# Kernel optimization log

Measured on AMD Instinct MI355X. Metric: run time of the kernel, lower is better.

## Reference

```python
import jax, jax.numpy as jnp
import numpy as np

N = 100000          # nodes
E = 1600000         # edges (nnz of A)
D_IN = 128
D_OUT = 128


def setup_inputs() -> dict:
    key = jax.random.key(0)
    ks = jax.random.split(key, 9)
    s = 1.0 / np.sqrt(D_IN)
    inp = {
        "h_n": jax.random.normal(ks[0], (N, D_IN), dtype=jnp.float32),
        "W_w": jax.random.uniform(ks[1], (D_OUT, D_IN), jnp.float32, -s, s),
        "W_b": jax.random.uniform(ks[2], (D_OUT,), jnp.float32, -s, s),
        "Wt_w": jax.random.uniform(ks[3], (D_OUT, D_IN), jnp.float32, -s, s),
        "Wt_b": jax.random.uniform(ks[4], (D_OUT,), jnp.float32, -s, s),
        "Ws_w": jax.random.uniform(ks[5], (D_OUT, D_IN), jnp.float32, -s, s),
        "Ws_b": jax.random.uniform(ks[6], (D_OUT,), jnp.float32, -s, s),
        # COO indices of sparse adjacency A (binary values): A[rows[e], cols[e]] = 1
        "rows": jax.random.randint(ks[7], (E,), 0, N, dtype=jnp.int64)
                if jax.config.jax_enable_x64 else
                jax.random.randint(ks[7], (E,), 0, N, dtype=jnp.int32),
        "cols": jax.random.randint(ks[8], (E,), 0, N, dtype=jnp.int32),
    }
    inp["rows"] = inp["rows"].astype(jnp.int32)
    return inp


def reference(h_n, W_w, W_b, Wt_w, Wt_b, Ws_w, Ws_b, rows, cols):
    # Dense projections: [N, D_OUT]
    Wh  = h_n @ W_w.T + W_b    # W(h_n)
    Wth = h_n @ Wt_w.T + Wt_b  # W_trans(h_n)
    Wsh = h_n @ Ws_w.T + Ws_b  # W_self(h_n)

    # A @ Wh  : out[i] = sum over edges (i=rows[e], j=cols[e]) of Wh[j]
    agg   = jax.ops.segment_sum(Wh[cols],  rows, num_segments=N)
    # A_T @ Wth : out[i] = sum over edges (j=rows[e], i=cols[e]) of Wth[j]
    agg_t = jax.ops.segment_sum(Wth[rows], cols, num_segments=N)

    # exact (erf-based) GELU, matching torch F.gelu default
    return jax.nn.gelu(agg + agg_t + Wsh, approximate=False)
```

## Files before the change

### kernel.cpp

```cpp
#include <hip/hip_runtime.h>


typedef __bf16 bf16;
typedef __bf16 bf16x2 __attribute__((ext_vector_type(2)));
typedef __bf16 bf16x4 __attribute__((ext_vector_type(4)));
typedef __bf16 bf16x8 __attribute__((ext_vector_type(8)));
typedef float  f32x4  __attribute__((ext_vector_type(4)));
typedef unsigned int u32;

#define D 128
#define BKT_CAP 2432
#define BIN_CHUNK 2048

__global__ void k_cast(const float* __restrict__ src, bf16* __restrict__ dst, int n4) {
    int i = blockIdx.x * 256 + threadIdx.x;
    if (i < n4) {
        f32x4 v = *(const f32x4*)&src[i * 4];
        bf16x4 o;
        o.x = (bf16)v.x; o.y = (bf16)v.y; o.z = (bf16)v.z; o.w = (bf16)v.w;
        *(bf16x4*)&dst[i * 4] = o;
    }
}

__global__ __launch_bounds__(256) void k_bin(
    const int* __restrict__ rows, const int* __restrict__ cols,
    int* __restrict__ gcnt_f, int* __restrict__ gcnt_r,
    u32* __restrict__ buf_f, u32* __restrict__ buf_r, int E, int B) {
    __shared__ int hf[1024], hr[1024];
    int t = threadIdx.x;
    int base = blockIdx.x * BIN_CHUNK;
    for (int b = t; b < B; b += 256) { hf[b] = 0; hr[b] = 0; }
    __syncthreads();
    int r[8], c[8];
#pragma unroll
    for (int i = 0; i < 8; ++i) {
        int e = base + i * 256 + t;
        if (e < E) {
            r[i] = rows[e]; c[i] = cols[e];
            atomicAdd(&hf[r[i] >> 7], 1);
            atomicAdd(&hr[c[i] >> 7], 1);
        }
    }
    __syncthreads();
    for (int b = t; b < B; b += 256) {
        int v = hf[b]; if (v) hf[b] = atomicAdd(&gcnt_f[b], v);
        int w = hr[b]; if (w) hr[b] = atomicAdd(&gcnt_r[b], w);
    }
    __syncthreads();
#pragma unroll
    for (int i = 0; i < 8; ++i) {
        int e = base + i * 256 + t;
        if (e < E) {
            int p = atomicAdd(&hf[r[i] >> 7], 1);
            if (p < BKT_CAP)
                buf_f[(size_t)(r[i] >> 7) * BKT_CAP + p] =
                    ((u32)(r[i] & 127) << 17) | (u32)c[i];
            int q = atomicAdd(&hr[c[i] >> 7], 1);
            if (q < BKT_CAP)
                buf_r[(size_t)(c[i] >> 7) * BKT_CAP + q] =
                    ((u32)(c[i] & 127) << 17) | (u32)r[i];
        }
    }
}

__global__ __launch_bounds__(256) void k_sort(
    const int* __restrict__ cnt_f, const int* __restrict__ cnt_r,
    u32* __restrict__ buf_f, u32* __restrict__ buf_r,
    int* __restrict__ off_f, int* __restrict__ off_r,
    int* __restrict__ deg_f, int* __restrict__ deg_r, int N) {
    __shared__ u32 words[BKT_CAP];
    __shared__ u32 sorted[BKT_CAP];
    __shared__ int hist[128], scn[128];
    int t = threadIdx.x, bkt = blockIdx.x;
    const int* cp; u32* buf; int* off; int* deg;
    if (blockIdx.y == 0) { cp = cnt_f; buf = buf_f + (size_t)bkt * BKT_CAP; off = off_f; deg = deg_f; }
    else                 { cp = cnt_r; buf = buf_r + (size_t)bkt * BKT_CAP; off = off_r; deg = deg_r; }
    int cnt = cp[bkt]; if (cnt > BKT_CAP) cnt = BKT_CAP;
    if (t < 128) hist[t] = 0;
    __syncthreads();
    for (int i = t; i < cnt; i += 256) {
        u32 w = buf[i]; words[i] = w;
        atomicAdd(&hist[w >> 17], 1);
    }
    __syncthreads();
    if (t < 128) scn[t] = hist[t];
    __syncthreads();
    for (int o = 1; o < 128; o <<= 1) {
        int v = (t < 128 && t >= o) ? scn[t - o] : 0;
        __syncthreads();
        if (t < 128) scn[t] += v;
        __syncthreads();
    }
    int node0 = bkt * 128;
    if (t < 128) {
        int start = scn[t] - hist[t];
        hist[t] = start;
        int node = node0 + t;
        if (node < N) { off[node] = bkt * BKT_CAP + start; deg[node] = scn[t] - start; }
    }
    __syncthreads();
    for (int i = t; i < cnt; i += 256) {
        u32 w = words[i];
        int p = atomicAdd(&hist[w >> 17], 1);
        sorted[p] = w & 0x1FFFF;
    }
    __syncthreads();
    for (int i = t; i < cnt; i += 256) buf[i] = sorted[i];
}

__global__ void k_agg(const bf16* __restrict__ h,
                      const int* __restrict__ off_f, const int* __restrict__ deg_f,
                      const u32* __restrict__ buf_f,
                      const int* __restrict__ off_r, const int* __restrict__ deg_r,
                      const u32* __restrict__ buf_r,
                      bf16* __restrict__ AH, bf16* __restrict__ ATH, int N) {
    int wave = threadIdx.x >> 6, lane = threadIdx.x & 63;
    int node = blockIdx.x * 4 + wave;
    if (node >= N) return;
    const int* off; const int* deg; const u32* idx; bf16* dst;
    if (blockIdx.y == 0) { off = off_f; deg = deg_f; idx = buf_f; dst = AH; }
    else                 { off = off_r; deg = deg_r; idx = buf_r; dst = ATH; }
    const bf16x2* h2 = (const bf16x2*)h;
    int p = off[node], end = p + deg[node];
    float ax0 = 0.f, ay0 = 0.f, ax1 = 0.f, ay1 = 0.f;
    float ax2 = 0.f, ay2 = 0.f, ax3 = 0.f, ay3 = 0.f;
    for (; p + 3 < end; p += 4) {
        u32 j0 = idx[p], j1 = idx[p + 1], j2 = idx[p + 2], j3 = idx[p + 3];
        bf16x2 v0 = h2[(size_t)j0 * 64 + lane];
        bf16x2 v1 = h2[(size_t)j1 * 64 + lane];
        bf16x2 v2 = h2[(size_t)j2 * 64 + lane];
        bf16x2 v3 = h2[(size_t)j3 * 64 + lane];
        ax0 += (float)v0.x; ay0 += (float)v0.y;
        ax1 += (float)v1.x; ay1 += (float)v1.y;
        ax2 += (float)v2.x; ay2 += (float)v2.y;
        ax3 += (float)v3.x; ay3 += (float)v3.y;
    }
    for (; p < end; ++p) {
        u32 j0 = idx[p];
        bf16x2 v0 = h2[(size_t)j0 * 64 + lane];
        ax0 += (float)v0.x; ay0 += (float)v0.y;
    }
    bf16x2 o;
    o.x = (bf16)((ax0 + ax1) + (ax2 + ax3));
    o.y = (bf16)((ay0 + ay1) + (ay2 + ay3));
    ((bf16x2*)dst)[(size_t)node * 64 + lane] = o;
}

__global__ __launch_bounds__(256) void k_gemm(
    const bf16* __restrict__ h, const bf16* __restrict__ AH, const bf16* __restrict__ ATH,
    const float* __restrict__ Ws_w, const float* __restrict__ W_w, const float* __restrict__ Wt_w,
    const float* __restrict__ Ws_b, const float* __restrict__ W_b, const float* __restrict__ Wt_b,
    const int* __restrict__ deg_out, const int* __restrict__ deg_in,
    float* __restrict__ out, int N) {
    __shared__ __align__(16) bf16 Ash[128 * 32];
    __shared__ __align__(16) bf16 Bsh[128 * 32];
    int t = threadIdx.x;
    int lane = t & 63;
    int w = t >> 6;
    int wm = (w >> 1) * 64, wn = (w & 1) * 64;
    int m0 = blockIdx.x * 128;

    f32x4 acc[4][4];
#pragma unroll
    for (int i = 0; i < 4; ++i)
#pragma unroll
        for (int j = 0; j < 4; ++j)
            acc[i][j] = (f32x4){0.f, 0.f, 0.f, 0.f};

    for (int kc = 0; kc < 12; ++kc) {
        const bf16*  X  = (kc < 4) ? h    : (kc < 8) ? AH  : ATH;
        const float* Wm = (kc < 4) ? Ws_w : (kc < 8) ? W_w : Wt_w;
        int c0 = (kc & 3) * 32;
#pragma unroll
        for (int r = 0; r < 2; ++r) {
            int v = r * 256 + t;
            int row = v >> 2, seg = v & 3;
            int xr = m0 + row; if (xr >= N) xr = N - 1;
            *(bf16x8*)&Ash[row * 32 + seg * 8] =
                *(const bf16x8*)&X[(size_t)xr * D + c0 + seg * 8];
        }
#pragma unroll
        for (int r = 0; r < 4; ++r) {
            int v = r * 256 + t;
            int row = v >> 3, seg = v & 7;
            f32x4 f = *(const f32x4*)&Wm[row * D + c0 + seg * 4];
            bf16x4 o;
            o.x = (bf16)f.x; o.y = (bf16)f.y; o.z = (bf16)f.z; o.w = (bf16)f.w;
            *(bf16x4*)&Bsh[row * 32 + seg * 4] = o;
        }
        __syncthreads();
        int kg = lane >> 4, lr = lane & 15;
        bf16x8 a[4], b[4];
#pragma unroll
        for (int i = 0; i < 4; ++i) {
            a[i] = *(const bf16x8*)&Ash[(wm + i * 16 + lr) * 32 + kg * 8];
            b[i] = *(const bf16x8*)&Bsh[(wn + i * 16 + lr) * 32 + kg * 8];
        }
#pragma unroll
        for (int i = 0; i < 4; ++i)
#pragma unroll
            for (int j = 0; j < 4; ++j)
                acc[i][j] = __builtin_amdgcn_mfma_f32_16x16x32_bf16(
                    a[i], b[j], acc[i][j], 0, 0, 0);
        __syncthreads();
    }

    int lr = lane & 15, lq = lane >> 4;
#pragma unroll
    for (int i = 0; i < 4; ++i) {
#pragma unroll
        for (int r = 0; r < 4; ++r) {
            int node = m0 + wm + i * 16 + lq * 4 + r;
            if (node >= N) continue;
            float fdr = (float)deg_out[node], fdc = (float)deg_in[node];
#pragma unroll
            for (int j = 0; j < 4; ++j) {
                int f = wn + j * 16 + lr;
                float val = acc[i][j][r] + Ws_b[f] + fdr * W_b[f] + fdc * Wt_b[f];
                float g = 0.5f * val * (1.0f + erff(val * 0.70710678118654752f));
                out[(size_t)node * D + f] = g;
            }
        }
    }
}

extern "C" void kernel_launch(void* const* d_in, const int* in_sizes, int n_in,
                              void* d_out, int out_size, void* d_ws, size_t ws_size,
                              hipStream_t stream) {
    const float* h    = (const float*)d_in[0];
    const float* W_w  = (const float*)d_in[1];
    const float* W_b  = (const float*)d_in[2];
    const float* Wt_w = (const float*)d_in[3];
    const float* Wt_b = (const float*)d_in[4];
    const float* Ws_w = (const float*)d_in[5];
    const float* Ws_b = (const float*)d_in[6];
    const int*   rows = (const int*)d_in[7];
    const int*   cols = (const int*)d_in[8];
    float* out = (float*)d_out;

    const int N = in_sizes[0] / D;
    const int E = in_sizes[7];
    const int B = (N + 127) >> 7;

    char* ws = (char*)d_ws;
    size_t off = 0;
    auto take = [&](size_t bytes) -> char* {
        char* p = ws + off;
        off += (bytes + 511) & ~(size_t)511;
        return p;
    };
    bf16* h_bf    = (bf16*)take((size_t)N * D * sizeof(bf16));
    bf16* AH      = (bf16*)take((size_t)N * D * sizeof(bf16));
    bf16* ATH     = (bf16*)take((size_t)N * D * sizeof(bf16));
    int*  gcnt    = (int*)take((size_t)2 * B * sizeof(int));
    int*  off_f   = (int*)take((size_t)N * sizeof(int));
    int*  off_r   = (int*)take((size_t)N * sizeof(int));
    int*  deg_f   = (int*)take((size_t)N * sizeof(int));
    int*  deg_r   = (int*)take((size_t)N * sizeof(int));
    u32*  buf_f   = (u32*)take((size_t)B * BKT_CAP * sizeof(u32));
    u32*  buf_r   = (u32*)take((size_t)B * BKT_CAP * sizeof(u32));
    int*  gcnt_f = gcnt, *gcnt_r = gcnt + B;

    hipMemsetAsync(gcnt, 0, (size_t)2 * B * sizeof(int), stream);

    int n4 = N * D / 4;
    k_cast<<<(n4 + 255) / 256, 256, 0, stream>>>(h, h_bf, n4);

    k_bin<<<(E + BIN_CHUNK - 1) / BIN_CHUNK, 256, 0, stream>>>(
        rows, cols, gcnt_f, gcnt_r, buf_f, buf_r, E, B);
    dim3 gsort(B, 2);
    k_sort<<<gsort, 256, 0, stream>>>(gcnt_f, gcnt_r, buf_f, buf_r,
                                      off_f, off_r, deg_f, deg_r, N);
    dim3 gagg((N + 3) / 4, 2);
    k_agg<<<gagg, 256, 0, stream>>>(h_bf, off_f, deg_f, buf_f,
                                    off_r, deg_r, buf_r, AH, ATH, N);
    k_gemm<<<B, 256, 0, stream>>>(h_bf, AH, ATH,
                                  Ws_w, W_w, Wt_w,
                                  Ws_b, W_b, Wt_b,
                                  deg_f, deg_r, out, N);
}
```

Measured before the change: 380.2 us.

## Locally sort edges in binning kernel and split aggregation across half-waves

The binning kernel now runs once per direction and handles larger edge chunks. It counting-sorts each chunk in shared memory and writes per-bucket runs contiguously, replacing the scattered global stores. The sort kernel pads each node's neighbour list to an even length using a zero row appended to h. This lets the aggregation kernel have each half-wave gather a different neighbour with 8-byte loads and combine the two halves with a shuffle. The cost is a serial per-bucket copy loop in the binning kernel, larger shared-memory use, and some wasted loads on padded zero entries.

```diff
diff --git a/kernel.cpp b/kernel.cpp
--- a/kernel.cpp
+++ b/kernel.cpp
@@ -2,15 +2,16 @@
 
 
 typedef __bf16 bf16;
-typedef __bf16 bf16x2 __attribute__((ext_vector_type(2)));
 typedef __bf16 bf16x4 __attribute__((ext_vector_type(4)));
 typedef __bf16 bf16x8 __attribute__((ext_vector_type(8)));
 typedef float  f32x4  __attribute__((ext_vector_type(4)));
 typedef unsigned int u32;
+typedef u32 u32x2 __attribute__((ext_vector_type(2)));
 
 #define D 128
-#define BKT_CAP 2432
-#define BIN_CHUNK 2048
+#define CAPC 2432
+#define SLAB 2560
+#define BIN_CHUNK 12544
 
 __global__ void k_cast(const float* __restrict__ src, bf16* __restrict__ dst, int n4) {
     int i = blockIdx.x * 256 + threadIdx.x;
@@ -26,39 +27,68 @@
     const int* __restrict__ rows, const int* __restrict__ cols,
     int* __restrict__ gcnt_f, int* __restrict__ gcnt_r,
     u32* __restrict__ buf_f, u32* __restrict__ buf_r, int E, int B) {
-    __shared__ int hf[1024], hr[1024];
+    __shared__ int hist[1024];
+    __shared__ int lbase[1024];
+    __shared__ int gbase[1024];
+    __shared__ int tsum[256];
+    __shared__ u32 sorted[BIN_CHUNK];
     int t = threadIdx.x;
+    int dir = blockIdx.y;
+    const int* key = dir ? cols : rows;
+    const int* pay = dir ? rows : cols;
+    int* gcnt = dir ? gcnt_r : gcnt_f;
+    u32* buf  = dir ? buf_r : buf_f;
     int base = blockIdx.x * BIN_CHUNK;
-    for (int b = t; b < B; b += 256) { hf[b] = 0; hr[b] = 0; }
-    __syncthreads();
-    int r[8], c[8];
-#pragma unroll
-    for (int i = 0; i < 8; ++i) {
+
+    for (int b = t; b < 1024; b += 256) hist[b] = 0;
+    __syncthreads();
+    for (int i = 0; i < BIN_CHUNK / 256; ++i) {
+        int e = base + i * 256 + t;
+        if (e < E) atomicAdd(&hist[key[e] >> 7], 1);
+    }
+    __syncthreads();
+    int s0 = hist[t * 4], s1 = hist[t * 4 + 1], s2 = hist[t * 4 + 2], s3 = hist[t * 4 + 3];
+    tsum[t] = s0 + s1 + s2 + s3;
+    __syncthreads();
+    for (int o = 1; o < 256; o <<= 1) {
+        int v = (t >= o) ? tsum[t - o] : 0;
+        __syncthreads();
+        tsum[t] += v;
+        __syncthreads();
+    }
+    int run = (t > 0) ? tsum[t - 1] : 0;
+    lbase[t * 4]     = run;
+    lbase[t * 4 + 1] = run + s0;
+    lbase[t * 4 + 2] = run + s0 + s1;
+    lbase[t * 4 + 3] = run + s0 + s1 + s2;
+    __syncthreads();
+    int total = tsum[255];
+    for (int b = t; b < 1024; b += 256) {
+        int nxt = (b < 1023) ? lbase[b + 1] : total;
+        int c = nxt - lbase[b];
+        gbase[b] = (c && b < B) ? atomicAdd(&gcnt[b], c) : 0;
+        hist[b] = lbase[b];
+    }
+    __syncthreads();
+    for (int i = 0; i < BIN_CHUNK / 256; ++i) {
         int e = base + i * 256 + t;
         if (e < E) {
-            r[i] = rows[e]; c[i] = cols[e];
-            atomicAdd(&hf[r[i] >> 7], 1);
-            atomicAdd(&hr[c[i] >> 7], 1);
+            int k = key[e], p = pay[e];
+            int pos = atomicAdd(&hist[k >> 7], 1);
+            sorted[pos] = ((u32)(k & 127) << 17) | (u32)p;
         }
     }
     __syncthreads();
     for (int b = t; b < B; b += 256) {
-        int v = hf[b]; if (v) hf[b] = atomicAdd(&gcnt_f[b], v);
-        int w = hr[b]; if (w) hr[b] = atomicAdd(&gcnt_r[b], w);
-    }
-    __syncthreads();
-#pragma unroll
-    for (int i = 0; i < 8; ++i) {
-        int e = base + i * 256 + t;
-        if (e < E) {
-            int p = atomicAdd(&hf[r[i] >> 7], 1);
-            if (p < BKT_CAP)
-                buf_f[(size_t)(r[i] >> 7) * BKT_CAP + p] =
-                    ((u32)(r[i] & 127) << 17) | (u32)c[i];
-            int q = atomicAdd(&hr[c[i] >> 7], 1);
-            if (q < BKT_CAP)
-                buf_r[(size_t)(c[i] >> 7) * BKT_CAP + q] =
-                    ((u32)(c[i] & 127) << 17) | (u32)r[i];
+        int lb = lbase[b];
+        int nxt = (b < 1023) ? lbase[b + 1] : total;
+        int c = nxt - lb;
+        if (!c) continue;
+        int gb = gbase[b];
+        u32* dst = buf + (size_t)b * SLAB;
+        for (int i = 0; i < c; ++i) {
+            int gp = gb + i;
+            if (gp < CAPC) dst[gp] = sorted[lb + i];
         }
     }
 }
@@ -67,15 +97,15 @@
     const int* __restrict__ cnt_f, const int* __restrict__ cnt_r,
     u32* __restrict__ buf_f, u32* __restrict__ buf_r,
     int* __restrict__ off_f, int* __restrict__ off_r,
-    int* __restrict__ deg_f, int* __restrict__ deg_r, int N) {
-    __shared__ u32 words[BKT_CAP];
-    __shared__ u32 sorted[BKT_CAP];
-    __shared__ int hist[128], scn[128];
+    int* __restrict__ deg_f, int* __restrict__ deg_r, int N, u32 PADV) {
+    __shared__ u32 words[CAPC];
+    __shared__ u32 sorted[SLAB];
+    __shared__ int hist[128], pscn[128], cur[128];
     int t = threadIdx.x, bkt = blockIdx.x;
     const int* cp; u32* buf; int* off; int* deg;
-    if (blockIdx.y == 0) { cp = cnt_f; buf = buf_f + (size_t)bkt * BKT_CAP; off = off_f; deg = deg_f; }
-    else                 { cp = cnt_r; buf = buf_r + (size_t)bkt * BKT_CAP; off = off_r; deg = deg_r; }
-    int cnt = cp[bkt]; if (cnt > BKT_CAP) cnt = BKT_CAP;
+    if (blockIdx.y == 0) { cp = cnt_f; buf = buf_f + (size_t)bkt * SLAB; off = off_f; deg = deg_f; }
+    else                 { cp = cnt_r; buf = buf_r + (size_t)bkt * SLAB; off = off_r; deg = deg_r; }
+    int cnt = cp[bkt]; if (cnt > CAPC) cnt = CAPC;
     if (t < 128) hist[t] = 0;
     __syncthreads();
     for (int i = t; i < cnt; i += 256) {
@@ -83,30 +113,37 @@
         atomicAdd(&hist[w >> 17], 1);
     }
     __syncthreads();
-    if (t < 128) scn[t] = hist[t];
+    int pd = 0;
+    if (t < 128) { pd = (hist[t] + 1) & ~1; pscn[t] = pd; }
     __syncthreads();
     for (int o = 1; o < 128; o <<= 1) {
-        int v = (t < 128 && t >= o) ? scn[t - o] : 0;
-        __syncthreads();
-        if (t < 128) scn[t] += v;
-        __syncthreads();
-    }
+        int v = (t < 128 && t >= o) ? pscn[t - o] : 0;
+        __syncthreads();
+        if (t < 128) pscn[t] += v;
+        __syncthreads();
+    }
+    int ptot = pscn[127];
     int node0 = bkt * 128;
     if (t < 128) {
-        int start = scn[t] - hist[t];
-        hist[t] = start;
+        int pstart = pscn[t] - pd;
+        cur[t] = pstart;
         int node = node0 + t;
-        if (node < N) { off[node] = bkt * BKT_CAP + start; deg[node] = scn[t] - start; }
-    }
+        if (node < N) { off[node] = bkt * SLAB + pstart; deg[node] = hist[t]; }
+    }
+    __syncthreads();
+    for (int i = t; i < ptot; i += 256) sorted[i] = PADV;
     __syncthreads();
     for (int i = t; i < cnt; i += 256) {
         u32 w = words[i];
-        int p = atomicAdd(&hist[w >> 17], 1);
+        int p = atomicAdd(&cur[w >> 17], 1);
         sorted[p] = w & 0x1FFFF;
     }
     __syncthreads();
-    for (int i = t; i < cnt; i += 256) buf[i] = sorted[i];
-}
+    for (int i = t; i < ptot; i += 256) buf[i] = sorted[i];
+}
+
+__device__ __forceinline__ float blo(u32 w) { return __uint_as_float(w << 16); }
+__device__ __forceinline__ float bhi(u32 w) { return __uint_as_float(w & 0xffff0000u); }
 
 __global__ void k_agg(const bf16* __restrict__ h,
                       const int* __restrict__ off_f, const int* __restrict__ deg_f,
@@ -120,30 +157,37 @@
     const int* off; const int* deg; const u32* idx; bf16* dst;
     if (blockIdx.y == 0) { off = off_f; deg = deg_f; idx = buf_f; dst = AH; }
     else                 { off = off_r; deg = deg_r; idx = buf_r; dst = ATH; }
-    const bf16x2* h2 = (const bf16x2*)h;
-    int p = off[node], end = p + deg[node];
-    float ax0 = 0.f, ay0 = 0.f, ax1 = 0.f, ay1 = 0.f;
-    float ax2 = 0.f, ay2 = 0.f, ax3 = 0.f, ay3 = 0.f;
-    for (; p + 3 < end; p += 4) {
-        u32 j0 = idx[p], j1 = idx[p + 1], j2 = idx[p + 2], j3 = idx[p + 3];
-        bf16x2 v0 = h2[(size_t)j0 * 64 + lane];
-        bf16x2 v1 = h2[(size_t)j1 * 64 + lane];
-        bf16x2 v2 = h2[(size_t)j2 * 64 + lane];
-        bf16x2 v3 = h2[(size_t)j3 * 64 + lane];
-        ax0 += (float)v0.x; ay0 += (float)v0.y;
-        ax1 += (float)v1.x; ay1 += (float)v1.y;
-        ax2 += (float)v2.x; ay2 += (float)v2.y;
-        ax3 += (float)v3.x; ay3 += (float)v3.y;
-    }
-    for (; p < end; ++p) {
-        u32 j0 = idx[p];
-        bf16x2 v0 = h2[(size_t)j0 * 64 + lane];
-        ax0 += (float)v0.x; ay0 += (float)v0.y;
-    }
-    bf16x2 o;
-    o.x = (bf16)((ax0 + ax1) + (ax2 + ax3));
-    o.y = (bf16)((ay0 + ay1) + (ay2 + ay3));
-    ((bf16x2*)dst)[(size_t)node * 64 + lane] = o;
+    int p = off[node];
+    int pend = p + ((deg[node] + 1) & ~1);
+    int half = lane >> 5, col = lane & 31;
+    const u32* h32 = (const u32*)h;
+    float a0 = 0.f, a1 = 0.f, a2 = 0.f, a3 = 0.f;
+    for (; p + 7 < pend; p += 8) {
+        u32 j[4];
+#pragma unroll
+        for (int u = 0; u < 4; ++u) j[u] = idx[p + 2 * u + half];
+#pragma unroll
+        for (int u = 0; u < 4; ++u) {
+            u32x2 w = *(const u32x2*)&h32[(size_t)j[u] * 64 + col * 2];
+            a0 += blo(w.x); a1 += bhi(w.x);
+            a2 += blo(w.y); a3 += bhi(w.y);
+        }
+    }
+    for (; p + 1 < pend; p += 2) {
+        u32 j = idx[p + half];
+        u32x2 w = *(const u32x2*)&h32[(size_t)j * 64 + col * 2];
+        a0 += blo(w.x); a1 += bhi(w.x);
+        a2 += blo(w.y); a3 += bhi(w.y);
+    }
+    a0 += __shfl_down(a0, 32);
+    a1 += __shfl_down(a1, 32);
+    a2 += __shfl_down(a2, 32);
+    a3 += __shfl_down(a3, 32);
+    if (half == 0) {
+        bf16x4 o;
+        o.x = (bf16)a0; o.y = (bf16)a1; o.z = (bf16)a2; o.w = (bf16)a3;
+        *(bf16x4*)&dst[(size_t)node * D + col * 4] = o;
+    }
 }
 
 __global__ __launch_bounds__(256) void k_gemm(
@@ -249,7 +293,7 @@
         off += (bytes + 511) & ~(size_t)511;
         return p;
     };
-    bf16* h_bf    = (bf16*)take((size_t)N * D * sizeof(bf16));
+    bf16* h_bf    = (bf16*)take((size_t)(N + 1) * D * sizeof(bf16));
     bf16* AH      = (bf16*)take((size_t)N * D * sizeof(bf16));
     bf16* ATH     = (bf16*)take((size_t)N * D * sizeof(bf16));
     int*  gcnt    = (int*)take((size_t)2 * B * sizeof(int));
@@ -257,20 +301,21 @@
     int*  off_r   = (int*)take((size_t)N * sizeof(int));
     int*  deg_f   = (int*)take((size_t)N * sizeof(int));
     int*  deg_r   = (int*)take((size_t)N * sizeof(int));
-    u32*  buf_f   = (u32*)take((size_t)B * BKT_CAP * sizeof(u32));
-    u32*  buf_r   = (u32*)take((size_t)B * BKT_CAP * sizeof(u32));
+    u32*  buf_f   = (u32*)take((size_t)B * SLAB * sizeof(u32));
+    u32*  buf_r   = (u32*)take((size_t)B * SLAB * sizeof(u32));
     int*  gcnt_f = gcnt, *gcnt_r = gcnt + B;
 
     hipMemsetAsync(gcnt, 0, (size_t)2 * B * sizeof(int), stream);
+    hipMemsetAsync(h_bf + (size_t)N * D, 0, D * sizeof(bf16), stream);
 
     int n4 = N * D / 4;
     k_cast<<<(n4 + 255) / 256, 256, 0, stream>>>(h, h_bf, n4);
 
-    k_bin<<<(E + BIN_CHUNK - 1) / BIN_CHUNK, 256, 0, stream>>>(
-        rows, cols, gcnt_f, gcnt_r, buf_f, buf_r, E, B);
+    dim3 gbin((E + BIN_CHUNK - 1) / BIN_CHUNK, 2);
+    k_bin<<<gbin, 256, 0, stream>>>(rows, cols, gcnt_f, gcnt_r, buf_f, buf_r, E, B);
     dim3 gsort(B, 2);
     k_sort<<<gsort, 256, 0, stream>>>(gcnt_f, gcnt_r, buf_f, buf_r,
-                                      off_f, off_r, deg_f, deg_r, N);
+                                      off_f, off_r, deg_f, deg_r, N, (u32)N);
     dim3 gagg((N + 3) / 4, 2);
     k_agg<<<gagg, 256, 0, stream>>>(h_bf, off_f, deg_f, buf_f,
                                     off_r, deg_r, buf_r, AH, ATH, N);
```

Result: faster. 347.8 us (-8.5%).
